# Kernel tuning notes

Measured on AMD Instinct MI355X. Metric: run time of the kernel, lower is better.

The kernel has to match this reference:

```python
import jax, jax.numpy as jnp
import numpy as np

N_HEADS = 16
LN_EPS = 1e-5

def layer_norm(x, w):
    # matches torch LayerNorm in fp32, weight-only (no bias)
    x = x.astype(jnp.float32)
    mu = jnp.mean(x, axis=-1, keepdims=True)
    var = jnp.mean((x - mu) ** 2, axis=-1, keepdims=True)
    return (x - mu) / jnp.sqrt(var + LN_EPS) * w

def rotate_half(t):
    t1, t2 = jnp.split(t, 2, axis=-1)
    return jnp.concatenate((-t2, t1), axis=-1)

def setup_inputs() -> dict:
    key = jax.random.key(0)
    ks = jax.random.split(key, 16)
    B, S, D, C = 2, 2048, 1024, 1024
    H = N_HEADS
    hd = D // H
    # rotary tables: emb = cat(freqs, freqs), freqs = t * inv_freq
    inv_freq = 1.0 / (10000.0 ** (np.arange(0, hd, 2, dtype=np.float32) / hd))
    t = np.arange(S, dtype=np.float32)
    freqs = np.outer(t, inv_freq)                       # [S, hd/2]
    emb = np.concatenate([freqs, freqs], axis=-1)       # [S, hd]
    s = 0.02
    return {
        "x": jax.random.normal(ks[0], (B, S, D), jnp.float32),
        "rotary_cos": jnp.asarray(np.cos(emb)),
        "rotary_sin": jnp.asarray(np.sin(emb)),
        "c": jax.random.normal(ks[1], (B, C), jnp.float32),
        "norm1_w": jnp.ones((D,), jnp.float32),
        "qkv_w": jax.random.normal(ks[2], (3 * D, D), jnp.float32) * s,
        "out_w": jax.random.normal(ks[3], (D, D), jnp.float32) * s,
        "norm2_w": jnp.ones((D,), jnp.float32),
        "fc1_w": jax.random.normal(ks[4], (4 * D, D), jnp.float32) * s,
        "fc1_b": jnp.zeros((4 * D,), jnp.float32),
        "fc2_w": jax.random.normal(ks[5], (D, 4 * D), jnp.float32) * s,
        "fc2_b": jnp.zeros((D,), jnp.float32),
        # NOTE: module zero-inits adaLN; random here for a non-degenerate baseline
        "ada_w": jax.random.normal(ks[6], (6 * D, C), jnp.float32) * s,
        "ada_b": jnp.zeros((6 * D,), jnp.float32),
    }

def reference(x, rotary_cos, rotary_sin, c, norm1_w, qkv_w, out_w, norm2_w,
              fc1_w, fc1_b, fc2_w, fc2_b, ada_w, ada_b):
    B, S, D = x.shape
    H = N_HEADS
    hd = D // H
    # AdaLN conditioning -> six [B,1,D] modulation tensors
    mods = (c @ ada_w.T + ada_b)[:, None, :]                       # [B,1,6D]
    shift_msa, scale_msa, gate_msa, shift_mlp, scale_mlp, gate_mlp = jnp.split(mods, 6, axis=2)
    x_skip = x
    # LN + modulate + QKV
    h = layer_norm(x, norm1_w) * (1.0 + scale_msa) + shift_msa     # [B,S,D]
    qkv = (h @ qkv_w.T).reshape(B, S, 3, H, hd)
    # rotary applied to packed qkv (q, k, and v) as in the torchscript fallback
    cos = rotary_cos[None, :, None, None, :]                       # [1,S,1,1,hd]
    sin = rotary_sin[None, :, None, None, :]
    qkv = qkv * cos + rotate_half(qkv) * sin
    q, k, v = qkv[:, :, 0], qkv[:, :, 1], qkv[:, :, 2]             # [B,S,H,hd]
    scale = hd ** -0.5
    scores = jnp.einsum('bqhd,bkhd->bhqk', q, k) * scale           # [B,H,S,S]
    attn = jax.nn.softmax(scores, axis=-1)
    o = jnp.einsum('bhqk,bkhd->bqhd', attn, v).reshape(B, S, D)
    # gated residual (dropout=0 / eval)
    x = gate_msa * (o @ out_w.T) + x_skip
    # second LN + modulate + MLP (exact gelu, matching F.gelu default)
    h2 = layer_norm(x, norm2_w) * (1.0 + scale_mlp) + shift_mlp
    mlp = jax.nn.gelu(h2 @ fc1_w.T + fc1_b, approximate=False) @ fc2_w.T + fc2_b
    return gate_mlp * mlp + x
```

## Files before the change

kernel.cpp:

```cpp
#include <hip/hip_runtime.h>
#include <hip/hip_bf16.h>


typedef unsigned short u16;
typedef unsigned int   u32;
typedef __bf16 bf16x8 __attribute__((ext_vector_type(8)));
typedef float  f32x4  __attribute__((ext_vector_type(4)));

#define MFMA_BF16(a, b, c) __builtin_amdgcn_mfma_f32_16x16x32_bf16((a), (b), (c), 0, 0, 0)

__device__ __forceinline__ float b2f(u16 u) {
    union { u32 i; float f; } v; v.i = ((u32)u) << 16; return v.f;
}
__device__ __forceinline__ u16 f2b(float f) {
    union { u32 i; float f; } v; v.f = f;
    u32 i = v.i;
    return (u16)((i + 0x7FFFu + ((i >> 16) & 1u)) >> 16);
}
__device__ __forceinline__ u32 pk2(float a, float b) {
#if __has_builtin(__builtin_amdgcn_cvt_pk_bf16_f32)
    typedef __bf16 bf16x2_t __attribute__((ext_vector_type(2)));
    union { bf16x2_t v; u32 u; } cv;
    cv.v = __builtin_amdgcn_cvt_pk_bf16_f32(a, b);
    return cv.u;
#else
    return (u32)f2b(a) | ((u32)f2b(b) << 16);
#endif
}
__device__ __forceinline__ float exp2_raw(float x) {
#if __has_builtin(__builtin_amdgcn_exp2f)
    return __builtin_amdgcn_exp2f(x);
#else
    float r;
    __asm("v_exp_f32 %0, %1" : "=v"(r) : "v"(x));
    return r;
#endif
}
__device__ __forceinline__ float finz(float v) {
    return __builtin_isfinite(v) ? v : 0.0f;
}
__device__ __forceinline__ void dma16(const void* g, void* l) {
    __builtin_amdgcn_global_load_lds(
        (const __attribute__((address_space(1))) unsigned int*)(uintptr_t)g,
        (__attribute__((address_space(3))) unsigned int*)(uintptr_t)l,
        16, 0, 0);
}

__device__ __forceinline__ void convert_body(
    const float* __restrict__ in, u16* __restrict__ out, int i, int kshift)
{
    size_t o = (size_t)i * 8;
    int bk   = (int)(o >> (kshift + 7));
    int rem  = (int)(o & (((size_t)128 << kshift) - 1));
    int kg   = rem >> 10;
    int nloc = (rem >> 3) & 127;
    const float* src = in + (((size_t)bk * 128 + nloc) << kshift) + kg * 8;
    float4 a = *(const float4*)src;
    float4 b = *(const float4*)(src + 4);
    union { u16 s[8]; float4 v; } wp;
    wp.s[0] = f2b(a.x); wp.s[1] = f2b(a.y); wp.s[2] = f2b(a.z); wp.s[3] = f2b(a.w);
    wp.s[4] = f2b(b.x); wp.s[5] = f2b(b.y); wp.s[6] = f2b(b.z); wp.s[7] = f2b(b.w);
    *(float4*)(out + o) = wp.v;
}

__global__ __launch_bounds__(256) void convert_kernel(
    const float* __restrict__ in, u16* __restrict__ out, int n8, int kshift)
{
    int i = blockIdx.x * 256 + threadIdx.x;
    if (i >= n8) return;
    convert_body(in, out, i, kshift);
}

__global__ __launch_bounds__(256) void convert2_kernel(
    const float* __restrict__ in0, u16* __restrict__ out0, int n80,
    const float* __restrict__ in1, u16* __restrict__ out1, int n81)
{
    int i = blockIdx.x * 256 + threadIdx.x;
    if (i < n80) {
        convert_body(in0, out0, i, 10);
    } else {
        i -= n80;
        if (i < n81) convert_body(in1, out1, i, 10);
    }
}

__global__ __launch_bounds__(64) void mods_kernel(
    const float* __restrict__ c, const float* __restrict__ ada_w,
    const float* __restrict__ ada_b, float* __restrict__ mods)
{
    const int n = blockIdx.x;
    const int lane = threadIdx.x;
    const float* wr = ada_w + (size_t)n * 1024;
    float a0 = 0.f, a1 = 0.f;
    for (int k = lane; k < 1024; k += 64) {
        float w = wr[k];
        a0 += w * c[k];
        a1 += w * c[1024 + k];
    }
    for (int o = 32; o > 0; o >>= 1) {
        a0 += __shfl_down(a0, o, 64);
        a1 += __shfl_down(a1, o, 64);
    }
    if (lane == 0) {
        float bb = ada_b[n];
        mods[n]        = a0 + bb;
        mods[6144 + n] = a1 + bb;
    }
}

__global__ __launch_bounds__(256) void ln_mod_kernel(
    const u16* __restrict__ xbf, const float* __restrict__ xf,
    const float* __restrict__ w, const float* __restrict__ mods,
    int scale_off, int shift_off, u16* __restrict__ out)
{
    const int row = blockIdx.x;
    const int b   = row >> 11;
    const int tid = threadIdx.x;
    const int wave = tid >> 6, lane = tid & 63;
    const size_t base = (size_t)row * 1024 + tid * 4;
    float v[4];
    if (xf) {
        float4 t = *(const float4*)(xf + base);
        v[0] = t.x; v[1] = t.y; v[2] = t.z; v[3] = t.w;
    } else {
        uint2 p = *(const uint2*)(xbf + base);
        union { u32 i; float f; } a, bb, cc, d;
        a.i  = p.x << 16;          v[0] = a.f;
        bb.i = p.x & 0xFFFF0000u;  v[1] = bb.f;
        cc.i = p.y << 16;          v[2] = cc.f;
        d.i  = p.y & 0xFFFF0000u;  v[3] = d.f;
    }
    float s  = v[0] + v[1] + v[2] + v[3];
    float sq = v[0]*v[0] + v[1]*v[1] + v[2]*v[2] + v[3]*v[3];
    #pragma unroll
    for (int o = 32; o > 0; o >>= 1) {
        s  += __shfl_down(s,  o, 64);
        sq += __shfl_down(sq, o, 64);
    }
    __shared__ float ws[8];
    if (lane == 0) { ws[wave] = s; ws[4 + wave] = sq; }
    __syncthreads();
    const float ts = (ws[0] + ws[1]) + (ws[2] + ws[3]);
    const float tq = (ws[4] + ws[5]) + (ws[6] + ws[7]);
    const float mean = ts * (1.0f / 1024.0f);
    const float var  = tq * (1.0f / 1024.0f) - mean * mean;
    const float inv  = rsqrtf(fmaxf(var, 0.f) + 1e-5f);
    union { u16 s4[4]; uint2 u2; } pk;
    for (int i = 0; i < 4; ++i) {
        int cidx = tid * 4 + i;
        float y = (v[i] - mean) * inv * w[cidx];
        y = y * (1.0f + mods[b * 6144 + scale_off + cidx]) + mods[b * 6144 + shift_off + cidx];
        pk.s4[i] = f2b(y);
    }
    size_t o = ((size_t)(row >> 7)) * 131072 + ((tid * 4) >> 3) * 1024
             + (row & 127) * 8 + ((tid * 4) & 7);
    *(uint2*)(out + o) = pk.u2;
}

template<int MODE, int TM>
__global__ __launch_bounds__(256) void gemm128(
    const u16* __restrict__ A, const u16* __restrict__ W,
    int M, int N, int K,
    const float* __restrict__ mods, const float* __restrict__ bias,
    const float* __restrict__ resid_f, const u16* __restrict__ resid_bf,
    float* __restrict__ out_f, u16* __restrict__ out_bf,
    u16* __restrict__ aux1, u16* __restrict__ aux2,
    const float* __restrict__ rcos, const float* __restrict__ rsin)
{
    constexpr int FI    = TM / 32;
    constexpr int WROWS = TM / 2;
    constexpr int ATILE = TM * 32;
    __shared__ u16 As[3][ATILE];
    __shared__ u16 Bs[3][4096];
    const int tid  = threadIdx.x;
    const int wave = tid >> 6, lane = tid & 63;
    const int quad = lane >> 4, l15 = lane & 15;
    const int wi = wave >> 1, wj = wave & 1;
    const int m0 = blockIdx.y * TM, n0 = blockIdx.x * 128;

    f32x4 acc[FI][4] = {};

    const u16* Asrc = A + (size_t)(m0 >> 7) * 128 * K + (m0 & 127) * 8
                        + wave * 1024 + lane * 8;
    const u16* Bsrc = W + (size_t)n0 * K + wave * 1024 + lane * 8;

    auto stage = [&](int tt, int buf) {
        const u16* a = Asrc + (size_t)tt * 4096;
        const u16* b = Bsrc + (size_t)tt * 4096;
        if constexpr (TM == 128) {
            dma16(a,       &As[buf][wave * 1024]);
            dma16(a + 512, &As[buf][wave * 1024 + 512]);
        } else {
            dma16(a, &As[buf][wave * 512]);
        }
        dma16(b,       &Bs[buf][wave * 1024]);
        dma16(b + 512, &Bs[buf][wave * 1024 + 512]);
    };

    const int nt = K >> 5;
    stage(0, 0);
    stage(1, 1);

    int cur = 0;
    for (int t = 0; t < nt; ++t) {
        if (t + 1 < nt) {
            if constexpr (TM == 128)
                __asm volatile("s_waitcnt vmcnt(4)" ::: "memory");
            else
                __asm volatile("s_waitcnt vmcnt(3)" ::: "memory");
        } else {
            __asm volatile("s_waitcnt vmcnt(0)" ::: "memory");
        }
        __builtin_amdgcn_s_barrier();
        if (t + 2 < nt) {
            int nb = cur + 2; if (nb >= 3) nb -= 3;
            stage(t + 2, nb);
        }
        bf16x8 af[FI], bw[4];
        #pragma unroll
        for (int f = 0; f < FI; ++f)
            af[f] = *(const bf16x8*)(&As[cur][quad * (TM * 8) + (wi * WROWS + f * 16 + l15) * 8]);
        #pragma unroll
        for (int f = 0; f < 4; ++f)
            bw[f] = *(const bf16x8*)(&Bs[cur][quad * 1024 + (wj * 64 + f * 16 + l15) * 8]);
        #pragma unroll
        for (int fi = 0; fi < FI; ++fi)
            #pragma unroll
            for (int fj = 0; fj < 4; ++fj)
                acc[fi][fj] = MFMA_BF16(af[fi], bw[fj], acc[fi][fj]);
        cur = (cur + 1 == 3) ? 0 : cur + 1;
    }

    if (MODE == 4) {
        const int colbase = n0 + wj * 64;
        const int wcol = colbase >> 10;
        const int hh   = (colbase & 1023) >> 6;
        #pragma unroll
        for (int fi = 0; fi < FI; ++fi) {
            const int rbase = m0 + wi * WROWS + fi * 16 + quad * 4;
            #pragma unroll
            for (int reg = 0; reg < 4; ++reg) {
                const int r = rbase + reg;
                const int b = r >> 11, s = r & 2047;
                const int bh = b * 16 + hh;
                #pragma unroll
                for (int fj = 0; fj < 2; ++fj) {
                    const int d2 = fj * 16 + l15;
                    float va = acc[fi][fj][reg];
                    float vb = acc[fi][fj + 2][reg];
                    float ca = rcos[s * 64 + d2];
                    float sa = rsin[s * 64 + d2];
                    float ra = va * ca - vb * sa;
                    float rb = vb * ca + va * sa;
                    if (wcol == 0) {
                        ra *= 0.18033688011f; rb *= 0.18033688011f;
                        u16* dst = aux1 + ((size_t)bh * 2048 + s) * 64;
                        dst[d2]      = f2b(ra);
                        dst[d2 + 32] = f2b(rb);
                    } else if (wcol == 1) {
                        size_t base = (size_t)bh * 131072 + (s >> 6) * 4096
                                    + (s & 63) * 8 + (d2 & 7);
                        aux2[base + (d2 >> 3) * 512]        = f2b(ra);
                        aux2[base + ((d2 >> 3) + 4) * 512]  = f2b(rb);
                    } else {
                        const int sl = s & 63;
                        const int sp = (sl & 32) | ((sl & 15) << 1) | ((sl >> 4) & 1);
                        size_t base = (size_t)bh * 131072 + (s >> 6) * 4096
                                    + (sp >> 3) * 512 + (sp & 7);
                        out_bf[base + d2 * 8]        = f2b(ra);
                        out_bf[base + (d2 + 32) * 8] = f2b(rb);
                    }
                }
            }
        }
        return;
    }

    #pragma unroll
    for (int fi = 0; fi < FI; ++fi) {
        #pragma unroll
        for (int fj = 0; fj < 4; ++fj) {
            const int cidx  = n0 + wj * 64 + fj * 16 + l15;
            const int rbase = m0 + wi * WROWS + fi * 16 + quad * 4;
            #pragma unroll
            for (int reg = 0; reg < 4; ++reg) {
                const int r = rbase + reg;
                float v = acc[fi][fj][reg];
                if (MODE == 1) {
                    float u = v + bias[cidx];
                    float g = 0.5f * u * (1.0f + erff(u * 0.70710678118654752f));
                    size_t o = ((size_t)(r >> 7)) * 524288 + (cidx >> 3) * 1024
                             + (r & 127) * 8 + (cidx & 7);
                    out_bf[o] = f2b(g);
                } else if (MODE == 2) {
                    int bb = r >> 11;
                    float gate = mods[bb * 6144 + 2048 + cidx];
                    out_bf[(size_t)r * N + cidx] = f2b(gate * v + resid_f[(size_t)r * N + cidx]);
                } else if (MODE == 3) {
                    int bb = r >> 11;
                    float u = v + bias[cidx];
                    float gate = mods[bb * 6144 + 5120 + cidx];
                    out_f[(size_t)r * N + cidx] =
                        finz(gate * u + b2f(resid_bf[(size_t)r * N + cidx]));
                }
            }
        }
    }
}

__global__ __launch_bounds__(512, 2) void attn_kernel(
    const u16* __restrict__ Q, const u16* __restrict__ Kb,
    const u16* __restrict__ Vb, u16* __restrict__ O)
{
    __shared__ u16 Ks[4096];
    __shared__ u16 Vs[4096];
    __shared__ u16 Ps[8][16 * 72];
    const int tid  = threadIdx.x;
    const int wave = tid >> 6, lane = tid & 63;
    const int quad = lane >> 4, l15 = lane & 15;
    const int bh = blockIdx.x & 31, qt = blockIdx.x >> 5;

    const u16* Qh = Q + ((size_t)bh * 2048 + qt * 128) * 64;

    const int soff = wave * 512 + lane * 8;
    const u16* kSrc = Kb + (size_t)bh * 131072 + soff;
    const u16* vSrc = Vb + (size_t)bh * 131072 + soff;
    u16* kDst = &Ks[wave * 512];
    u16* vDst = &Vs[wave * 512];

    bf16x8 aq[2];
    #pragma unroll
    for (int kh = 0; kh < 2; ++kh)
        aq[kh] = *(const bf16x8*)(Qh + (size_t)(wave * 16 + l15) * 64 + kh * 32 + quad * 8);

    f32x4 acc_o[4] = {};
    float lsum[4] = {0.f, 0.f, 0.f, 0.f};

    for (int kb = 0; kb < 32; ++kb) {
        __syncthreads();
        dma16(kSrc, kDst);
        dma16(vSrc, vDst);
        kSrc += 4096; vSrc += 4096;
        __syncthreads();

        f32x4 sc[4] = {};
        #pragma unroll
        for (int kt = 0; kt < 4; ++kt)
            #pragma unroll
            for (int kh = 0; kh < 2; ++kh) {
                bf16x8 bk = *(const bf16x8*)(&Ks[(quad + kh * 4) * 512 + (kt * 16 + l15) * 8]);
                sc[kt] = MFMA_BF16(aq[kh], bk, sc[kt]);
            }

        #pragma unroll
        for (int kt = 0; kt < 4; ++kt)
            #pragma unroll
            for (int reg = 0; reg < 4; ++reg)
                sc[kt][reg] = exp2_raw(fminf(sc[kt][reg], 72.f));
        #pragma unroll
        for (int reg = 0; reg < 4; ++reg)
            lsum[reg] += (sc[0][reg] + sc[1][reg]) + (sc[2][reg] + sc[3][reg]);

        #pragma unroll
        for (int reg = 0; reg < 4; ++reg) {
            u32* prow = (u32*)(&Ps[wave][(quad * 4 + reg) * 72]);
            prow[l15]      = pk2(sc[0][reg], sc[1][reg]);
            prow[16 + l15] = pk2(sc[2][reg], sc[3][reg]);
        }
        __asm volatile("s_waitcnt lgkmcnt(0)" ::: "memory");

        bf16x8 ap0 = *(const bf16x8*)(&Ps[wave][l15 * 72 + quad * 8]);
        bf16x8 ap1 = *(const bf16x8*)(&Ps[wave][l15 * 72 + 32 + quad * 8]);
        #pragma unroll
        for (int dt = 0; dt < 4; ++dt) {
            bf16x8 bv0 = *(const bf16x8*)(&Vs[quad * 512 + (dt * 16 + l15) * 8]);
            bf16x8 bv1 = *(const bf16x8*)(&Vs[(quad + 4) * 512 + (dt * 16 + l15) * 8]);
            acc_o[dt] = MFMA_BF16(ap0, bv0, acc_o[dt]);
            acc_o[dt] = MFMA_BF16(ap1, bv1, acc_o[dt]);
        }
    }

    float linv[4];
    #pragma unroll
    for (int reg = 0; reg < 4; ++reg) {
        float l = lsum[reg];
        l += __shfl_xor(l, 1, 64);
        l += __shfl_xor(l, 2, 64);
        l += __shfl_xor(l, 4, 64);
        l += __shfl_xor(l, 8, 64);
        linv[reg] = 1.0f / l;
    }

    const int b = bh >> 4, hh = bh & 15;
    #pragma unroll
    for (int dt = 0; dt < 4; ++dt)
        #pragma unroll
        for (int reg = 0; reg < 4; ++reg) {
            int q = qt * 128 + wave * 16 + quad * 4 + reg;
            int r = b * 2048 + q;
            int col = hh * 64 + dt * 16 + l15;
            float v = acc_o[dt][reg] * linv[reg];
            O[((size_t)(r >> 7)) * 131072 + (col >> 3) * 1024
              + (r & 127) * 8 + (col & 7)] = f2b(v);
        }
}

extern "C" void kernel_launch(void* const* d_in, const int* in_sizes, int n_in,
                              void* d_out, int out_size, void* d_ws, size_t ws_size,
                              hipStream_t stream)
{
    const float* x     = (const float*)d_in[0];
    const float* rcos  = (const float*)d_in[1];
    const float* rsin  = (const float*)d_in[2];
    const float* c     = (const float*)d_in[3];
    const float* n1w   = (const float*)d_in[4];
    const float* qkvw  = (const float*)d_in[5];
    const float* outw  = (const float*)d_in[6];
    const float* n2w   = (const float*)d_in[7];
    const float* fc1w  = (const float*)d_in[8];
    const float* fc1b  = (const float*)d_in[9];
    const float* fc2w  = (const float*)d_in[10];
    const float* fc2b  = (const float*)d_in[11];
    const float* adaw  = (const float*)d_in[12];
    const float* adab  = (const float*)d_in[13];
    float* out = (float*)d_out;

    char* ws = (char*)d_ws;
    const size_t MB8 = (size_t)8 * 1024 * 1024;
    float* mods  = (float*)ws;
    u16*   W     = (u16*)(ws + 49152);
    char*  S1    = ws + 49152 + MB8;
    char*  S2    = S1 + MB8;

    u16* h    = (u16*)d_out;
    u16* qs   = (u16*)S1;
    u16* ks   = (u16*)S2;
    u16* vT   = (u16*)(S2 + MB8);
    u16* ob   = (u16*)d_out;
    u16* x2   = (u16*)S1;
    u16* h2   = (u16*)d_out;
    u16* mid  = (u16*)S2;
    u16* Wo   = W + 3145728;

    mods_kernel<<<6144, 64, 0, stream>>>(c, adaw, adab, mods);
    ln_mod_kernel<<<4096, 256, 0, stream>>>(nullptr, x, n1w, mods, 1024, 0, h);
    convert2_kernel<<<2048, 256, 0, stream>>>(qkvw, W, 393216, outw, Wo, 131072);
    gemm128<4, 128><<<dim3(24, 32), 256, 0, stream>>>(h, W, 4096, 3072, 1024,
        nullptr, nullptr, nullptr, nullptr, nullptr, vT, qs, ks, rcos, rsin);
    attn_kernel<<<512, 512, 0, stream>>>(qs, ks, vT, ob);
    gemm128<2, 64><<<dim3(8, 64), 256, 0, stream>>>(ob, Wo, 4096, 1024, 1024,
        mods, nullptr, x, nullptr, nullptr, x2, nullptr, nullptr, nullptr, nullptr);
    ln_mod_kernel<<<4096, 256, 0, stream>>>(x2, nullptr, n2w, mods, 4096, 3072, h2);
    convert_kernel<<<2048, 256, 0, stream>>>(fc1w, W, 524288, 10);
    gemm128<1, 128><<<dim3(32, 32), 256, 0, stream>>>(h2, W, 4096, 4096, 1024,
        nullptr, fc1b, nullptr, nullptr, nullptr, mid, nullptr, nullptr, nullptr, nullptr);
    convert_kernel<<<2048, 256, 0, stream>>>(fc2w, W, 524288, 12);
    gemm128<3, 64><<<dim3(8, 64), 256, 0, stream>>>(mid, W, 4096, 1024, 4096,
        mods, fc2b, nullptr, x2, out, nullptr, nullptr, nullptr, nullptr, nullptr);
}
```

Measured before the change: 412.2 us.

## Compute transposed scores so P feeds PV MFMA from registers without LDS

Swaps the MFMA operands in the QK^T product so each lane holds the scores for one query row across keys. The packed bf16 probabilities can then serve directly as the A operand of the PV MFMA, which removes the per-wave LDS staging buffer, its writes, the wait and the reads. The V permutation in the QKV epilogue is changed so the key ordering matches this register layout. The row-sum reduction is rewritten to use cross-quad shuffles plus a broadcast, and correctness depends on the permuted V layout exactly matching the MFMA output lane mapping.

```diff
diff --git a/kernel.cpp b/kernel.cpp
--- a/kernel.cpp
+++ b/kernel.cpp
@@ -6,6 +6,7 @@
 typedef unsigned int   u32;
 typedef __bf16 bf16x8 __attribute__((ext_vector_type(8)));
 typedef float  f32x4  __attribute__((ext_vector_type(4)));
+typedef u32    u32x4  __attribute__((ext_vector_type(4)));
 
 #define MFMA_BF16(a, b, c) __builtin_amdgcn_mfma_f32_16x16x32_bf16((a), (b), (c), 0, 0, 0)
 
@@ -264,7 +265,8 @@
                         aux2[base + ((d2 >> 3) + 4) * 512]  = f2b(rb);
                     } else {
                         const int sl = s & 63;
-                        const int sp = (sl & 32) | ((sl & 15) << 1) | ((sl >> 4) & 1);
+                        const int sp = (sl & 32) | ((sl & 12) << 1)
+                                     | ((sl & 16) >> 2) | (sl & 3);
                         size_t base = (size_t)bh * 131072 + (s >> 6) * 4096
                                     + (sp >> 3) * 512 + (sp & 7);
                         out_bf[base + d2 * 8]        = f2b(ra);
@@ -314,7 +316,6 @@
 {
     __shared__ u16 Ks[4096];
     __shared__ u16 Vs[4096];
-    __shared__ u16 Ps[8][16 * 72];
     const int tid  = threadIdx.x;
     const int wave = tid >> 6, lane = tid & 63;
     const int quad = lane >> 4, l15 = lane & 15;
@@ -334,7 +335,7 @@
         aq[kh] = *(const bf16x8*)(Qh + (size_t)(wave * 16 + l15) * 64 + kh * 32 + quad * 8);
 
     f32x4 acc_o[4] = {};
-    float lsum[4] = {0.f, 0.f, 0.f, 0.f};
+    float lsum = 0.f;
 
     for (int kb = 0; kb < 32; ++kb) {
         __syncthreads();
@@ -349,7 +350,7 @@
             #pragma unroll
             for (int kh = 0; kh < 2; ++kh) {
                 bf16x8 bk = *(const bf16x8*)(&Ks[(quad + kh * 4) * 512 + (kt * 16 + l15) * 8]);
-                sc[kt] = MFMA_BF16(aq[kh], bk, sc[kt]);
+                sc[kt] = MFMA_BF16(bk, aq[kh], sc[kt]);
             }
 
         #pragma unroll
@@ -358,40 +359,37 @@
             for (int reg = 0; reg < 4; ++reg)
                 sc[kt][reg] = exp2_raw(fminf(sc[kt][reg], 72.f));
         #pragma unroll
-        for (int reg = 0; reg < 4; ++reg)
-            lsum[reg] += (sc[0][reg] + sc[1][reg]) + (sc[2][reg] + sc[3][reg]);
-
-        #pragma unroll
-        for (int reg = 0; reg < 4; ++reg) {
-            u32* prow = (u32*)(&Ps[wave][(quad * 4 + reg) * 72]);
-            prow[l15]      = pk2(sc[0][reg], sc[1][reg]);
-            prow[16 + l15] = pk2(sc[2][reg], sc[3][reg]);
-        }
-        __asm volatile("s_waitcnt lgkmcnt(0)" ::: "memory");
-
-        bf16x8 ap0 = *(const bf16x8*)(&Ps[wave][l15 * 72 + quad * 8]);
-        bf16x8 ap1 = *(const bf16x8*)(&Ps[wave][l15 * 72 + 32 + quad * 8]);
+        for (int kt = 0; kt < 4; ++kt)
+            lsum += (sc[kt][0] + sc[kt][1]) + (sc[kt][2] + sc[kt][3]);
+
+        union { u32x4 u; bf16x8 v; } ap0, ap1;
+        ap0.u[0] = pk2(sc[0][0], sc[0][1]);
+        ap0.u[1] = pk2(sc[0][2], sc[0][3]);
+        ap0.u[2] = pk2(sc[1][0], sc[1][1]);
+        ap0.u[3] = pk2(sc[1][2], sc[1][3]);
+        ap1.u[0] = pk2(sc[2][0], sc[2][1]);
+        ap1.u[1] = pk2(sc[2][2], sc[2][3]);
+        ap1.u[2] = pk2(sc[3][0], sc[3][1]);
+        ap1.u[3] = pk2(sc[3][2], sc[3][3]);
+
         #pragma unroll
         for (int dt = 0; dt < 4; ++dt) {
             bf16x8 bv0 = *(const bf16x8*)(&Vs[quad * 512 + (dt * 16 + l15) * 8]);
             bf16x8 bv1 = *(const bf16x8*)(&Vs[(quad + 4) * 512 + (dt * 16 + l15) * 8]);
-            acc_o[dt] = MFMA_BF16(ap0, bv0, acc_o[dt]);
-            acc_o[dt] = MFMA_BF16(ap1, bv1, acc_o[dt]);
-        }
-    }
-
+            acc_o[dt] = MFMA_BF16(ap0.v, bv0, acc_o[dt]);
+            acc_o[dt] = MFMA_BF16(ap1.v, bv1, acc_o[dt]);
+        }
+    }
+
+    lsum += __shfl_xor(lsum, 16, 64);
+    lsum += __shfl_xor(lsum, 32, 64);
+    const float linv_q = 1.0f / lsum;
+
+    const int b = bh >> 4, hh = bh & 15;
     float linv[4];
     #pragma unroll
-    for (int reg = 0; reg < 4; ++reg) {
-        float l = lsum[reg];
-        l += __shfl_xor(l, 1, 64);
-        l += __shfl_xor(l, 2, 64);
-        l += __shfl_xor(l, 4, 64);
-        l += __shfl_xor(l, 8, 64);
-        linv[reg] = 1.0f / l;
-    }
-
-    const int b = bh >> 4, hh = bh & 15;
+    for (int reg = 0; reg < 4; ++reg)
+        linv[reg] = __shfl(linv_q, quad * 4 + reg, 16);
     #pragma unroll
     for (int dt = 0; dt < 4; ++dt)
         #pragma unroll
```

Result: faster. 402.4 us (-2.4%).
